# Optimization experiments

Measured on AMD Instinct MI355X. Metric: run time of the kernel, lower is better.

Reference implementation:

```python
import jax, jax.numpy as jnp
import numpy as np

N_NODES = 40000
N_EDGES = 150000
H, D = 4, 128  # heads, per-head dim (h_feats=512)


def _edge_softmax(e, dst, n):
    # e: [E, H] attention logits; softmax over edges sharing a dst node
    m = jax.ops.segment_max(e, dst, num_segments=n)
    w = jnp.exp(e - m[dst])
    s = jax.ops.segment_sum(w, dst, num_segments=n)
    return w / s[dst]


def _gat_conv(x, src, dst, W, al, ar, b, activate):
    # DGL GATConv: feat = x @ W -> [N, H, D]
    n = x.shape[0]
    feat = (x @ W).reshape(n, H, D)
    el = jnp.einsum('nhd,hd->nh', feat, al)  # [N, H]
    er = jnp.einsum('nhd,hd->nh', feat, ar)
    e = jax.nn.leaky_relu(el[src] + er[dst], negative_slope=0.2)  # [E, H]
    a = _edge_softmax(e, dst, n)
    msg = feat[src] * a[:, :, None]  # [E, H, D]
    out = jax.ops.segment_sum(msg, dst, num_segments=n)  # [N, H, D]
    out = out + b.reshape(1, H, D)
    if activate:
        out = jax.nn.leaky_relu(out, negative_slope=0.01)  # F.leaky_relu default
    return out


def _hetero_layer(h, edges, W, al, ar, b, activate):
    # HeteroGraphConv with aggregate='sum' over edge types, then flatten heads
    n = h.shape[0]
    out = jnp.zeros((n, H, D), h.dtype)
    for t, (src, dst) in enumerate(edges):
        out = out + _gat_conv(h, src, dst, W[t], al[t], ar[t], b[t], activate)
    return out.reshape(n, H * D)


def setup_inputs() -> dict:
    key = jax.random.key(0)
    ks = jax.random.split(key, 20)
    inp = {}
    inp['x'] = jax.random.normal(ks[0], (N_NODES, 1024), jnp.float32)
    for i, nm in enumerate(['src0', 'dst0', 'src1', 'dst1']):
        inp[nm] = jax.random.randint(ks[1 + i], (N_EDGES,), 0, N_NODES, jnp.int32)
    def wscale(k, shape, fan_in):
        return jax.random.normal(k, shape, jnp.float32) * (1.0 / np.sqrt(fan_in))
    inp['W0'] = wscale(ks[5], (2, 1024, 512), 1024)
    inp['al0'] = wscale(ks[6], (2, H, D), D)
    inp['ar0'] = wscale(ks[7], (2, H, D), D)
    inp['b0'] = jnp.zeros((2, 512), jnp.float32)
    inp['W1'] = wscale(ks[8], (2, 512, 512), 512)
    inp['al1'] = wscale(ks[9], (2, H, D), D)
    inp['ar1'] = wscale(ks[10], (2, H, D), D)
    inp['b1'] = jnp.zeros((2, 512), jnp.float32)
    inp['W2'] = wscale(ks[11], (2, 512, 512), 512)
    inp['al2'] = wscale(ks[12], (2, H, D), D)
    inp['ar2'] = wscale(ks[13], (2, H, D), D)
    inp['b2'] = jnp.zeros((2, 512), jnp.float32)
    inp['Wout'] = wscale(ks[14], (512, 2983), 512)
    inp['bout'] = jnp.zeros((2983,), jnp.float32)
    return inp


def reference(x, src0, dst0, src1, dst1,
              W0, al0, ar0, b0, W1, al1, ar1, b1, W2, al2, ar2, b2,
              Wout, bout):
    edges = [(src0, dst0), (src1, dst1)]
    h = _hetero_layer(x, edges, W0, al0, ar0, b0, activate=True)
    h = _hetero_layer(h, edges, W1, al1, ar1, b1, activate=True)
    h = _hetero_layer(h, edges, W2, al2, ar2, b2, activate=False)
    return h @ Wout + bout
```

## Files before the change

### kernel.cpp

```cpp
#include <hip/hip_runtime.h>
#include <hip/hip_bf16.h>

#define NN 40000
#define NE 150000
#define HF 512
#define NHEAD 4

typedef __bf16 bf16x8 __attribute__((ext_vector_type(8)));
typedef float floatx4 __attribute__((ext_vector_type(4)));
typedef __hip_bfloat16 bf16;
typedef unsigned short u16;

__device__ __forceinline__ float bf2f(bf16 v) { return __bfloat162float(v); }

__device__ __forceinline__ void gload16(const void* g, void* l) {
    __builtin_amdgcn_global_load_lds(
        (const __attribute__((address_space(1))) void*)g,
        (__attribute__((address_space(3))) void*)l, 16, 0, 0);
}

__device__ __forceinline__ void wait_vm0() {
    asm volatile("s_waitcnt vmcnt(0)" ::: "memory");
}

__global__ void cast_k(const float* __restrict__ in, bf16* __restrict__ out, int n) {
    int i = (blockIdx.x * blockDim.x + threadIdx.x) * 8;
    if (i + 7 < n) {
        float4 v0 = *(const float4*)(in + i);
        float4 v1 = *(const float4*)(in + i + 4);
        union { uint4 u; u16 s[8]; } w;
        float fv[8] = {v0.x, v0.y, v0.z, v0.w, v1.x, v1.y, v1.z, v1.w};
#pragma unroll
        for (int j = 0; j < 8; j++) {
            bf16 b = __float2bfloat16(fv[j]);
            w.s[j] = *(const u16*)&b;
        }
        *(uint4*)(out + i) = w.u;
    } else {
        for (int j = i; j < n; j++) out[j] = __float2bfloat16(in[j]);
    }
}

__global__ void transpose_k(const float* __restrict__ W, bf16* __restrict__ WT,
                            int K, int Nn) {
    __shared__ float tile[32][33];
    int n0 = blockIdx.x * 32, k0 = blockIdx.y * 32;
    int tx = threadIdx.x, ty = threadIdx.y;
    int n = n0 + tx, k = k0 + ty;
    if (n < Nn && k < K) tile[ty][tx] = W[(size_t)k * Nn + n];
    __syncthreads();
    int nn = n0 + ty, kk = k0 + tx;
    if (nn < Nn && kk < K) WT[(size_t)nn * K + kk] = __float2bfloat16(tile[tx][ty]);
}

template <bool HAS_BIAS>
__global__ __launch_bounds__(256) void gemm_k(const bf16* __restrict__ A,
                                              const bf16* __restrict__ BT,
                                              float* __restrict__ C,
                                              const float* __restrict__ bias,
                                              int M, int Nn, int K) {
    __shared__ __align__(16) unsigned short As[2][128][32];
    __shared__ __align__(16) unsigned short Bs[2][128][32];

    const int nwg = gridDim.x * gridDim.y;
    const int orig = blockIdx.y * gridDim.x + blockIdx.x;
    const int qq = nwg >> 3, r8 = nwg & 7;
    const int xcd = orig & 7, loc = orig >> 3;
    const int swz = (xcd < r8 ? xcd * (qq + 1) : r8 * (qq + 1) + (xcd - r8) * qq) + loc;
    const int ntile = swz % gridDim.x;
    const int mtile = swz / gridDim.x;
    const int m0 = mtile * 128;
    const int n0 = ntile * 128;

    const int t = threadIdx.x;
    const int lane = t & 63;
    const int wave = t >> 6;
    const int wm = wave >> 1, wn = wave & 1;
    const int q = lane >> 4, r = lane & 15;

    const int srow = wave * 32 + (lane >> 2);
    const int scol = ((lane & 3) ^ ((srow >> 1) & 3)) * 8;
    int ar0 = m0 + srow;        if (ar0 >= M)  ar0 = M - 1;
    int ar1 = m0 + srow + 16;   if (ar1 >= M)  ar1 = M - 1;
    int br0 = n0 + srow;        if (br0 >= Nn) br0 = Nn - 1;
    int br1 = n0 + srow + 16;   if (br1 >= Nn) br1 = Nn - 1;
    const unsigned short* Ag0 = (const unsigned short*)A + (size_t)ar0 * K + scol;
    const unsigned short* Ag1 = (const unsigned short*)A + (size_t)ar1 * K + scol;
    const unsigned short* Bg0 = (const unsigned short*)BT + (size_t)br0 * K + scol;
    const unsigned short* Bg1 = (const unsigned short*)BT + (size_t)br1 * K + scol;
    unsigned short* Alb[2] = {&As[0][0][0] + wave * 1024, &As[1][0][0] + wave * 1024};
    unsigned short* Blb[2] = {&Bs[0][0][0] + wave * 1024, &Bs[1][0][0] + wave * 1024};

    const int rchunk = (q ^ ((r >> 1) & 3)) * 8;

    floatx4 acc[4][4] = {};
    const int nt = K >> 5;
    int cur = 0;
    gload16(Ag0, Alb[0]);
    gload16(Ag1, Alb[0] + 512);
    gload16(Bg0, Blb[0]);
    gload16(Bg1, Blb[0] + 512);
    wait_vm0();
    __syncthreads();
    for (int tt = 0; tt < nt; tt++) {
        if (tt + 1 < nt) {
            const int k1 = (tt + 1) << 5;
            gload16(Ag0 + k1, Alb[cur ^ 1]);
            gload16(Ag1 + k1, Alb[cur ^ 1] + 512);
            gload16(Bg0 + k1, Blb[cur ^ 1]);
            gload16(Bg1 + k1, Blb[cur ^ 1] + 512);
        }
        bf16x8 a[4], b[4];
#pragma unroll
        for (int i = 0; i < 4; i++)
            a[i] = *(const bf16x8*)&As[cur][wm * 64 + i * 16 + r][rchunk];
#pragma unroll
        for (int j = 0; j < 4; j++)
            b[j] = *(const bf16x8*)&Bs[cur][wn * 64 + j * 16 + r][rchunk];
#pragma unroll
        for (int i = 0; i < 4; i++)
#pragma unroll
            for (int j = 0; j < 4; j++)
                acc[i][j] = __builtin_amdgcn_mfma_f32_16x16x32_bf16(a[i], b[j], acc[i][j], 0, 0, 0);
        wait_vm0();
        __syncthreads();
        cur ^= 1;
    }

    float bv4[4] = {0.f, 0.f, 0.f, 0.f};
    if (HAS_BIAS) {
#pragma unroll
        for (int j = 0; j < 4; j++) {
            int col = n0 + wn * 64 + j * 16 + r;
            if (col < Nn) bv4[j] = bias[col];
        }
    }
#pragma unroll
    for (int i = 0; i < 4; i++)
#pragma unroll
        for (int j = 0; j < 4; j++)
#pragma unroll
            for (int rr = 0; rr < 4; rr++) {
                int row = m0 + wm * 64 + i * 16 + q * 4 + rr;
                int col = n0 + wn * 64 + j * 16 + r;
                if (row < M && col < Nn) {
                    float v = acc[i][j][rr];
                    if (HAS_BIAS) v += bv4[j];
                    C[(size_t)row * Nn + col] = v;
                }
            }
}

__global__ void attn_k(const float* __restrict__ feat, const float* __restrict__ al,
                       const float* __restrict__ ar, float* __restrict__ el,
                       float* __restrict__ er) {
    int lane = threadIdx.x & 63;
    int wave = threadIdx.x >> 6;
    int node = blockIdx.x * 4 + wave;
    if (node >= NN) return;
    int h = lane >> 4;
    const float* fp = feat + (size_t)node * HF + lane * 8;
    float4 f0 = *(const float4*)fp;
    float4 f1 = *(const float4*)(fp + 4);
    const float* alp = al + h * 128 + (lane & 15) * 8;
    const float* arp = ar + h * 128 + (lane & 15) * 8;
    float fv[8] = {f0.x, f0.y, f0.z, f0.w, f1.x, f1.y, f1.z, f1.w};
    float sl = 0.f, sr = 0.f;
#pragma unroll
    for (int j = 0; j < 8; j++) {
        sl += fv[j] * alp[j];
        sr += fv[j] * arp[j];
    }
#pragma unroll
    for (int off = 8; off >= 1; off >>= 1) {
        sl += __shfl_down(sl, off, 16);
        sr += __shfl_down(sr, off, 16);
    }
    if ((lane & 15) == 0) {
        el[node * NHEAD + h] = sl;
        er[node * NHEAD + h] = sr;
    }
}

__global__ void deg_count_k(const int* __restrict__ dst, int* __restrict__ deg) {
    int e = blockIdx.x * blockDim.x + threadIdx.x;
    if (e < NE) atomicAdd(&deg[dst[e]], 1);
}

__global__ void scan_k(const int* __restrict__ deg, int* __restrict__ off) {
    __shared__ int part[1024];
    const int CH = (NN + 1023) >> 10;
    int t = threadIdx.x;
    int base = t * CH;
    int s = 0;
    for (int i = 0; i < CH; i++) {
        int idx = base + i;
        if (idx < NN) s += deg[idx];
    }
    part[t] = s;
    __syncthreads();
    for (int d = 1; d < 1024; d <<= 1) {
        int v = (t >= d) ? part[t - d] : 0;
        __syncthreads();
        part[t] += v;
        __syncthreads();
    }
    int run = (t == 0) ? 0 : part[t - 1];
    for (int i = 0; i < CH; i++) {
        int idx = base + i;
        if (idx < NN) {
            off[idx] = run;
            run += deg[idx];
        } else if (idx == NN) {
            off[NN] = run;
        }
    }
}

__global__ void fill_k(const int* __restrict__ src, const int* __restrict__ dst,
                       const int* __restrict__ off, int* __restrict__ cur,
                       int* __restrict__ csrc) {
    int e = blockIdx.x * blockDim.x + threadIdx.x;
    if (e >= NE) return;
    int d = dst[e];
    int p = atomicAdd(&cur[d], 1);
    csrc[off[d] + p] = src[e];
}

__global__ __launch_bounds__(256) void gather_k(
    const int* __restrict__ off, const int* __restrict__ csrc,
    const float* __restrict__ el, const float* __restrict__ er,
    const float* __restrict__ feat, const float* __restrict__ bt,
    bf16* __restrict__ hout, int first, int act) {
    int lane = threadIdx.x & 63;
    int wave = threadIdx.x >> 6;
    int d = blockIdx.x * 4 + wave;
    if (d >= NN) return;
    int h = lane >> 4;
    int o0 = off[d], o1 = off[d + 1];
    float erd = er[d * NHEAD + h];

    float m = -3.0e38f, sum = 0.f;
    for (int i = o0; i < o1; i++) {
        int s = csrc[i];
        float lg = el[s * NHEAD + h] + erd;
        lg = lg > 0.f ? lg : 0.2f * lg;
        float mn = fmaxf(m, lg);
        sum = sum * __expf(m - mn) + __expf(lg - mn);
        m = mn;
    }
    float inv = sum > 0.f ? 1.f / sum : 0.f;
    float acc[8] = {};
    for (int i = o0; i < o1; i++) {
        int s = csrc[i];
        float lg = el[s * NHEAD + h] + erd;
        lg = lg > 0.f ? lg : 0.2f * lg;
        float a = __expf(lg - m) * inv;
        const float* fp = feat + (size_t)s * HF + lane * 8;
        float4 f0 = *(const float4*)fp;
        float4 f1 = *(const float4*)(fp + 4);
        acc[0] += f0.x * a;
        acc[1] += f0.y * a;
        acc[2] += f0.z * a;
        acc[3] += f0.w * a;
        acc[4] += f1.x * a;
        acc[5] += f1.y * a;
        acc[6] += f1.z * a;
        acc[7] += f1.w * a;
    }
    const float* bp = bt + lane * 8;
    float4 b0 = *(const float4*)bp;
    float4 b1 = *(const float4*)(bp + 4);
    float bv[8] = {b0.x, b0.y, b0.z, b0.w, b1.x, b1.y, b1.z, b1.w};
    u16* hp = (u16*)(hout + (size_t)d * HF + lane * 8);
    union U8 { uint4 v; u16 s[8]; };
    U8 prev;
    if (!first) prev.v = *(const uint4*)hp;
    U8 outw;
#pragma unroll
    for (int j = 0; j < 8; j++) {
        float v = acc[j] + bv[j];
        if (act) v = v > 0.f ? v : 0.01f * v;
        if (!first) {
            bf16 pb = *(const bf16*)&prev.s[j];
            v += bf2f(pb);
        }
        bf16 ob = __float2bfloat16(v);
        outw.s[j] = *(const u16*)&ob;
    }
    *(uint4*)hp = outw.v;
}

extern "C" void kernel_launch(void* const* d_in, const int* in_sizes, int n_in,
                              void* d_out, int out_size, void* d_ws, size_t ws_size,
                              hipStream_t stream) {
    const float* x = (const float*)d_in[0];
    const int* srcs[2] = {(const int*)d_in[1], (const int*)d_in[3]};
    const int* dsts[2] = {(const int*)d_in[2], (const int*)d_in[4]};
    const float* W[3] = {(const float*)d_in[5], (const float*)d_in[9], (const float*)d_in[13]};
    const float* al[3] = {(const float*)d_in[6], (const float*)d_in[10], (const float*)d_in[14]};
    const float* ar[3] = {(const float*)d_in[7], (const float*)d_in[11], (const float*)d_in[15]};
    const float* bb[3] = {(const float*)d_in[8], (const float*)d_in[12], (const float*)d_in[16]};
    const float* Wout = (const float*)d_in[17];
    const float* bout = (const float*)d_in[18];

    char* ws = (char*)d_ws;
    size_t off = 0;
    auto walloc = [&](size_t bytes) {
        void* p = ws + off;
        off = (off + bytes + 255) & ~(size_t)255;
        return p;
    };
    bf16* h0 = (bf16*)walloc((size_t)NN * HF * 2);
    bf16* h1 = (bf16*)walloc((size_t)NN * HF * 2);
    float* feat = (float*)walloc((size_t)NN * HF * 4);
    float* el = (float*)walloc((size_t)NN * NHEAD * 4);
    float* er = (float*)walloc((size_t)NN * NHEAD * 4);
    bf16* WT = (bf16*)walloc((size_t)2983 * 512 * 2);
    int* deg = (int*)walloc((size_t)NN * 4);
    int* cur = (int*)walloc((size_t)NN * 4);
    int* offs[2];
    int* csrc[2];
    for (int t = 0; t < 2; t++) {
        offs[t] = (int*)walloc((size_t)(NN + 1) * 4);
        csrc[t] = (int*)walloc((size_t)NE * 4);
    }

    bf16* xb = (bf16*)((char*)d_out + (size_t)NN * HF * 4);

    cast_k<<<(NN * 1024 / 8 + 255) / 256, 256, 0, stream>>>(x, xb, NN * 1024);

    const int EB = (NE + 255) / 256;
    for (int t = 0; t < 2; t++) {
        hipMemsetAsync(deg, 0, (size_t)NN * 4, stream);
        hipMemsetAsync(cur, 0, (size_t)NN * 4, stream);
        deg_count_k<<<EB, 256, 0, stream>>>(dsts[t], deg);
        scan_k<<<1, 1024, 0, stream>>>(deg, offs[t]);
        fill_k<<<EB, 256, 0, stream>>>(srcs[t], dsts[t], offs[t], cur, csrc[t]);
    }

    const int MT = (NN + 127) / 128;

    for (int l = 0; l < 3; l++) {
        const int K = (l == 0) ? 1024 : 512;
        const bf16* hin = (l == 0) ? xb : ((l == 1) ? h0 : h1);
        bf16* hout = (l == 0) ? h0 : ((l == 1) ? h1 : h0);
        const int act = (l < 2) ? 1 : 0;
        for (int t = 0; t < 2; t++) {
            transpose_k<<<dim3(512 / 32, K / 32), dim3(32, 32), 0, stream>>>(
                W[l] + (size_t)t * K * 512, WT, K, 512);
            gemm_k<false><<<dim3(512 / 128, MT), 256, 0, stream>>>(
                hin, WT, feat, nullptr, NN, 512, K);
            attn_k<<<NN / 4, 256, 0, stream>>>(feat, al[l] + t * HF, ar[l] + t * HF, el, er);
            gather_k<<<NN / 4, 256, 0, stream>>>(offs[t], csrc[t], el, er, feat,
                                                 bb[l] + t * HF, hout, t == 0 ? 1 : 0, act);
        }
    }

    transpose_k<<<dim3((2983 + 31) / 32, 512 / 32), dim3(32, 32), 0, stream>>>(
        Wout, WT, 512, 2983);
    gemm_k<true><<<dim3((2983 + 127) / 128, MT), 256, 0, stream>>>(
        h0, WT, (float*)d_out, bout, NN, 2983, 512);
}
```

Before: 1.700 ms.

## Batch both edge-type projections into one GEMM with bf16 features and fused gather

Result: faster. 1.578 ms (-7.1%).

```diff
diff --git a/kernel.cpp b/kernel.cpp
--- a/kernel.cpp
+++ b/kernel.cpp
@@ -12,6 +12,7 @@
 typedef unsigned short u16;
 
 __device__ __forceinline__ float bf2f(bf16 v) { return __bfloat162float(v); }
+__device__ __forceinline__ float u2f(u16 v) { return __uint_as_float(((unsigned)v) << 16); }
 
 __device__ __forceinline__ void gload16(const void* g, void* l) {
     __builtin_amdgcn_global_load_lds(
@@ -22,6 +23,9 @@
 __device__ __forceinline__ void wait_vm0() {
     asm volatile("s_waitcnt vmcnt(0)" ::: "memory");
 }
+
+__device__ __forceinline__ void store_c(float* p, float v) { *p = v; }
+__device__ __forceinline__ void store_c(bf16* p, float v) { *p = __float2bfloat16(v); }
 
 __global__ void cast_k(const float* __restrict__ in, bf16* __restrict__ out, int n) {
     int i = (blockIdx.x * blockDim.x + threadIdx.x) * 8;
@@ -53,10 +57,10 @@
     if (nn < Nn && kk < K) WT[(size_t)nn * K + kk] = __float2bfloat16(tile[tx][ty]);
 }
 
-template <bool HAS_BIAS>
+template <typename TOUT, bool HAS_BIAS>
 __global__ __launch_bounds__(256) void gemm_k(const bf16* __restrict__ A,
                                               const bf16* __restrict__ BT,
-                                              float* __restrict__ C,
+                                              TOUT* __restrict__ C,
                                               const float* __restrict__ bias,
                                               int M, int Nn, int K) {
     __shared__ __align__(16) unsigned short As[2][128][32];
@@ -146,39 +150,47 @@
                 if (row < M && col < Nn) {
                     float v = acc[i][j][rr];
                     if (HAS_BIAS) v += bv4[j];
-                    C[(size_t)row * Nn + col] = v;
+                    store_c(&C[(size_t)row * Nn + col], v);
                 }
             }
 }
 
-__global__ void attn_k(const float* __restrict__ feat, const float* __restrict__ al,
-                       const float* __restrict__ ar, float* __restrict__ el,
+__global__ void attn_k(const bf16* __restrict__ featb, const float* __restrict__ al_l,
+                       const float* __restrict__ ar_l, float* __restrict__ el,
                        float* __restrict__ er) {
     int lane = threadIdx.x & 63;
     int wave = threadIdx.x >> 6;
     int node = blockIdx.x * 4 + wave;
     if (node >= NN) return;
-    int h = lane >> 4;
-    const float* fp = feat + (size_t)node * HF + lane * 8;
-    float4 f0 = *(const float4*)fp;
-    float4 f1 = *(const float4*)(fp + 4);
-    const float* alp = al + h * 128 + (lane & 15) * 8;
-    const float* arp = ar + h * 128 + (lane & 15) * 8;
-    float fv[8] = {f0.x, f0.y, f0.z, f0.w, f1.x, f1.y, f1.z, f1.w};
+    int tt = lane >> 5, h = (lane >> 3) & 3, ld = lane & 7;
+    const u16* fp = (const u16*)featb + (size_t)node * 1024 + lane * 16;
+    union { uint4 v; u16 s[8]; } u0, u1;
+    u0.v = *(const uint4*)fp;
+    u1.v = *(const uint4*)(fp + 8);
+    const float* alp = al_l + tt * HF + h * 128 + ld * 16;
+    const float* arp = ar_l + tt * HF + h * 128 + ld * 16;
     float sl = 0.f, sr = 0.f;
 #pragma unroll
     for (int j = 0; j < 8; j++) {
-        sl += fv[j] * alp[j];
-        sr += fv[j] * arp[j];
-    }
-#pragma unroll
-    for (int off = 8; off >= 1; off >>= 1) {
-        sl += __shfl_down(sl, off, 16);
-        sr += __shfl_down(sr, off, 16);
-    }
-    if ((lane & 15) == 0) {
-        el[node * NHEAD + h] = sl;
-        er[node * NHEAD + h] = sr;
+        float f = u2f(u0.s[j]);
+        sl += f * alp[j];
+        sr += f * arp[j];
+    }
+#pragma unroll
+    for (int j = 0; j < 8; j++) {
+        float f = u2f(u1.s[j]);
+        sl += f * alp[8 + j];
+        sr += f * arp[8 + j];
+    }
+#pragma unroll
+    for (int off = 4; off >= 1; off >>= 1) {
+        sl += __shfl_down(sl, off, 8);
+        sr += __shfl_down(sr, off, 8);
+    }
+    if (ld == 0) {
+        size_t o = (size_t)tt * NN * NHEAD + node * NHEAD + h;
+        el[o] = sl;
+        er[o] = sr;
     }
 }
 
@@ -228,67 +240,67 @@
 }
 
 __global__ __launch_bounds__(256) void gather_k(
-    const int* __restrict__ off, const int* __restrict__ csrc,
+    const int* __restrict__ off0, const int* __restrict__ csrc0,
+    const int* __restrict__ off1, const int* __restrict__ csrc1,
     const float* __restrict__ el, const float* __restrict__ er,
-    const float* __restrict__ feat, const float* __restrict__ bt,
-    bf16* __restrict__ hout, int first, int act) {
+    const bf16* __restrict__ featb, const float* __restrict__ bb_l,
+    bf16* __restrict__ hout, int act) {
     int lane = threadIdx.x & 63;
     int wave = threadIdx.x >> 6;
     int d = blockIdx.x * 4 + wave;
     if (d >= NN) return;
     int h = lane >> 4;
-    int o0 = off[d], o1 = off[d + 1];
-    float erd = er[d * NHEAD + h];
-
-    float m = -3.0e38f, sum = 0.f;
-    for (int i = o0; i < o1; i++) {
-        int s = csrc[i];
-        float lg = el[s * NHEAD + h] + erd;
-        lg = lg > 0.f ? lg : 0.2f * lg;
-        float mn = fmaxf(m, lg);
-        sum = sum * __expf(m - mn) + __expf(lg - mn);
-        m = mn;
-    }
-    float inv = sum > 0.f ? 1.f / sum : 0.f;
-    float acc[8] = {};
-    for (int i = o0; i < o1; i++) {
-        int s = csrc[i];
-        float lg = el[s * NHEAD + h] + erd;
-        lg = lg > 0.f ? lg : 0.2f * lg;
-        float a = __expf(lg - m) * inv;
-        const float* fp = feat + (size_t)s * HF + lane * 8;
-        float4 f0 = *(const float4*)fp;
-        float4 f1 = *(const float4*)(fp + 4);
-        acc[0] += f0.x * a;
-        acc[1] += f0.y * a;
-        acc[2] += f0.z * a;
-        acc[3] += f0.w * a;
-        acc[4] += f1.x * a;
-        acc[5] += f1.y * a;
-        acc[6] += f1.z * a;
-        acc[7] += f1.w * a;
-    }
-    const float* bp = bt + lane * 8;
-    float4 b0 = *(const float4*)bp;
-    float4 b1 = *(const float4*)(bp + 4);
-    float bv[8] = {b0.x, b0.y, b0.z, b0.w, b1.x, b1.y, b1.z, b1.w};
-    u16* hp = (u16*)(hout + (size_t)d * HF + lane * 8);
-    union U8 { uint4 v; u16 s[8]; };
-    U8 prev;
-    if (!first) prev.v = *(const uint4*)hp;
-    U8 outw;
+    const int* offs[2] = {off0, off1};
+    const int* csrcs[2] = {csrc0, csrc1};
+
+    float out[8] = {};
+#pragma unroll
+    for (int tt = 0; tt < 2; tt++) {
+        const int* off = offs[tt];
+        const int* csrc = csrcs[tt];
+        const float* elt = el + (size_t)tt * NN * NHEAD;
+        int o0 = off[d], o1 = off[d + 1];
+        float erd = er[(size_t)tt * NN * NHEAD + d * NHEAD + h];
+        float m = -3.0e38f, sum = 0.f;
+        for (int i = o0; i < o1; i++) {
+            int s = csrc[i];
+            float lg = elt[s * NHEAD + h] + erd;
+            lg = lg > 0.f ? lg : 0.2f * lg;
+            float mn = fmaxf(m, lg);
+            sum = sum * __expf(m - mn) + __expf(lg - mn);
+            m = mn;
+        }
+        float inv = sum > 0.f ? 1.f / sum : 0.f;
+        float acc[8] = {};
+        for (int i = o0; i < o1; i++) {
+            int s = csrc[i];
+            float lg = elt[s * NHEAD + h] + erd;
+            lg = lg > 0.f ? lg : 0.2f * lg;
+            float a = __expf(lg - m) * inv;
+            const u16* fp = (const u16*)featb + (size_t)s * 1024 + tt * HF + lane * 8;
+            union { uint4 v; u16 s8[8]; } u;
+            u.v = *(const uint4*)fp;
+#pragma unroll
+            for (int j = 0; j < 8; j++) acc[j] += u2f(u.s8[j]) * a;
+        }
+        const float* bp = bb_l + tt * HF + lane * 8;
+        float4 b0 = *(const float4*)bp;
+        float4 b1 = *(const float4*)(bp + 4);
+        float bv[8] = {b0.x, b0.y, b0.z, b0.w, b1.x, b1.y, b1.z, b1.w};
+#pragma unroll
+        for (int j = 0; j < 8; j++) {
+            float v = acc[j] + bv[j];
+            if (act) v = v > 0.f ? v : 0.01f * v;
+            out[j] += v;
+        }
+    }
+    union { uint4 v; u16 s[8]; } outw;
 #pragma unroll
     for (int j = 0; j < 8; j++) {
-        float v = acc[j] + bv[j];
-        if (act) v = v > 0.f ? v : 0.01f * v;
-        if (!first) {
-            bf16 pb = *(const bf16*)&prev.s[j];
-            v += bf2f(pb);
-        }
-        bf16 ob = __float2bfloat16(v);
+        bf16 ob = __float2bfloat16(out[j]);
         outw.s[j] = *(const u16*)&ob;
     }
-    *(uint4*)hp = outw.v;
+    *(uint4*)((u16*)hout + (size_t)d * HF + lane * 8) = outw.v;
 }
 
 extern "C" void kernel_launch(void* const* d_in, const int* in_sizes, int n_in,
@@ -313,10 +325,10 @@
     };
     bf16* h0 = (bf16*)walloc((size_t)NN * HF * 2);
     bf16* h1 = (bf16*)walloc((size_t)NN * HF * 2);
-    float* feat = (float*)walloc((size_t)NN * HF * 4);
-    float* el = (float*)walloc((size_t)NN * NHEAD * 4);
-    float* er = (float*)walloc((size_t)NN * NHEAD * 4);
+    float* el = (float*)walloc((size_t)2 * NN * NHEAD * 4);
+    float* er = (float*)walloc((size_t)2 * NN * NHEAD * 4);
     bf16* WT = (bf16*)walloc((size_t)2983 * 512 * 2);
+    bf16* WT2 = (bf16*)walloc((size_t)1024 * 1024 * 2);
     int* deg = (int*)walloc((size_t)NN * 4);
     int* cur = (int*)walloc((size_t)NN * 4);
     int* offs[2];
@@ -327,6 +339,7 @@
     }
 
     bf16* xb = (bf16*)((char*)d_out + (size_t)NN * HF * 4);
+    bf16* featb = (bf16*)((char*)d_out + (size_t)NN * HF * 4 + (size_t)NN * 1024 * 2);
 
     cast_k<<<(NN * 1024 / 8 + 255) / 256, 256, 0, stream>>>(x, xb, NN * 1024);
 
@@ -346,19 +359,18 @@
         const bf16* hin = (l == 0) ? xb : ((l == 1) ? h0 : h1);
         bf16* hout = (l == 0) ? h0 : ((l == 1) ? h1 : h0);
         const int act = (l < 2) ? 1 : 0;
-        for (int t = 0; t < 2; t++) {
+        for (int t = 0; t < 2; t++)
             transpose_k<<<dim3(512 / 32, K / 32), dim3(32, 32), 0, stream>>>(
-                W[l] + (size_t)t * K * 512, WT, K, 512);
-            gemm_k<false><<<dim3(512 / 128, MT), 256, 0, stream>>>(
-                hin, WT, feat, nullptr, NN, 512, K);
-            attn_k<<<NN / 4, 256, 0, stream>>>(feat, al[l] + t * HF, ar[l] + t * HF, el, er);
-            gather_k<<<NN / 4, 256, 0, stream>>>(offs[t], csrc[t], el, er, feat,
-                                                 bb[l] + t * HF, hout, t == 0 ? 1 : 0, act);
-        }
+                W[l] + (size_t)t * K * 512, WT2 + (size_t)t * 512 * K, K, 512);
+        gemm_k<bf16, false><<<dim3(1024 / 128, MT), 256, 0, stream>>>(
+            hin, WT2, featb, nullptr, NN, 1024, K);
+        attn_k<<<NN / 4, 256, 0, stream>>>(featb, al[l], ar[l], el, er);
+        gather_k<<<NN / 4, 256, 0, stream>>>(offs[0], csrc[0], offs[1], csrc[1],
+                                             el, er, featb, bb[l], hout, act);
     }
 
     transpose_k<<<dim3((2983 + 31) / 32, 512 / 32), dim3(32, 32), 0, stream>>>(
         Wout, WT, 512, 2983);
-    gemm_k<true><<<dim3((2983 + 127) / 128, MT), 256, 0, stream>>>(
+    gemm_k<float, true><<<dim3((2983 + 127) / 128, MT), 256, 0, stream>>>(
         h0, WT, (float*)d_out, bout, NN, 2983, 512);
 }
```
